# Kernel optimization log

Measured on AMD Instinct MI355X. Metric: run time of the kernel, lower is better.

The kernel has to match this reference:

```python
import jax, jax.numpy as jnp
import numpy as np

B, S, D, H = 2, 2048, 1024, 16
HD = D // H  # head_dim = 64
NEG = -1.0e9


def setup_inputs() -> dict:
    key = jax.random.key(0)
    ks = jax.random.split(key, 6)
    scale = 1.0 / np.sqrt(D)
    x = jax.random.normal(ks[0], (B, S, D), dtype=jnp.float32)
    # causal additive mask: 1.0 where position is masked (future), matching scores += mask * -1e9
    mask = jnp.triu(jnp.ones((S, S), dtype=jnp.float32), k=1)[None, None, :, :]
    wq = jax.random.normal(ks[1], (D, D), dtype=jnp.float32) * scale
    wk = jax.random.normal(ks[2], (D, D), dtype=jnp.float32) * scale
    wv = jax.random.normal(ks[3], (D, D), dtype=jnp.float32) * scale
    wo = jax.random.normal(ks[4], (D, D), dtype=jnp.float32) * scale
    z = jnp.zeros((D,), dtype=jnp.float32)
    return {"x": x, "mask": mask, "wq": wq, "bq": z, "wk": wk, "bk": z,
            "wv": wv, "bv": z, "wo": wo, "bo": z}


def _split_heads(t):
    # [B, S, D] -> [B, H, S, HD]
    return t.reshape(B, S, H, HD).transpose(0, 2, 1, 3)


def reference(x, mask, wq, bq, wk, bk, wv, bv, wo, bo):
    q = _split_heads(x @ wq + bq)
    k = _split_heads(x @ wk + bk)
    v = _split_heads(x @ wv + bv)
    inv_sqrt_d = 1.0 / jnp.sqrt(jnp.float32(HD))
    scores = jnp.einsum("bhqd,bhkd->bhqk", q, k) * inv_sqrt_d
    scores = scores + mask * NEG
    attn = jax.nn.softmax(scores, axis=-1)
    out = jnp.einsum("bhqk,bhkd->bhqd", attn, v)
    out = out.transpose(0, 2, 1, 3).reshape(B, S, D)  # merge heads
    return out @ wo + bo
```

## Files before the change

### kernel.cpp

```cpp
#include <hip/hip_runtime.h>
#include <hip/hip_bf16.h>


typedef __bf16 bf16x8 __attribute__((ext_vector_type(8)));
typedef __bf16 bf16x4 __attribute__((ext_vector_type(4)));
typedef float f32x4 __attribute__((ext_vector_type(4)));

#define S_LEN 2048
#define DMODEL 1024
#define NHEAD 16
#define HDIM 64
#define MROWS 4096

#define AS1 __attribute__((address_space(1)))
#define AS3 __attribute__((address_space(3)))

#define QSCALE 0.18033688f
#define LDP 136

__global__ void cast_x_kernel(const float* __restrict__ X, __bf16* __restrict__ Xb) {
    int i = (blockIdx.x * blockDim.x + threadIdx.x) * 4;
    float4 f = *(const float4*)&X[i];
    Xb[i + 0] = (__bf16)f.x;
    Xb[i + 1] = (__bf16)f.y;
    Xb[i + 2] = (__bf16)f.z;
    Xb[i + 3] = (__bf16)f.w;
}

__global__ void transpose_cast_kernel(
    const float* __restrict__ W0, const float* __restrict__ W1,
    const float* __restrict__ W2, const float* __restrict__ W3,
    __bf16* __restrict__ T0, __bf16* __restrict__ T1,
    __bf16* __restrict__ T2, __bf16* __restrict__ T3) {
    const float* W = (blockIdx.z == 0) ? W0 : (blockIdx.z == 1) ? W1 : (blockIdx.z == 2) ? W2 : W3;
    __bf16* WT = (blockIdx.z == 0) ? T0 : (blockIdx.z == 1) ? T1 : (blockIdx.z == 2) ? T2 : T3;
    __shared__ float tile[32][33];
    int bx = blockIdx.x, by = blockIdx.y;
    int tx = threadIdx.x;
    for (int i = threadIdx.y; i < 32; i += 8)
        tile[i][tx] = W[(size_t)(by * 32 + i) * DMODEL + bx * 32 + tx];
    __syncthreads();
    for (int i = threadIdx.y; i < 32; i += 8)
        WT[(size_t)(bx * 32 + i) * DMODEL + by * 32 + tx] = (__bf16)tile[tx][i];
}

__global__ __launch_bounds__(256) void gemm_qkv_kernel(
    const __bf16* __restrict__ X,
    const __bf16* __restrict__ WqT, const __bf16* __restrict__ WkT, const __bf16* __restrict__ WvT,
    const float* __restrict__ bq, const float* __restrict__ bk, const float* __restrict__ bv,
    __bf16* __restrict__ Q, __bf16* __restrict__ K, __bf16* __restrict__ Vt) {
    const int which = blockIdx.z;
    const __bf16* Bt = (which == 0) ? WqT : (which == 1) ? WkT : WvT;
    const float* bias = (which == 0) ? bq : (which == 1) ? bk : bv;
    __bf16* Out = (which == 0) ? Q : (which == 1) ? K : Vt;

    __shared__ alignas(16) __bf16 As[128 * 64];
    __shared__ alignas(16) __bf16 Bs[64 * 64];

    const int tid = threadIdx.x;
    const int lane = tid & 63;
    const int wave = tid >> 6;
    const int wm = wave >> 1, wn = wave & 1;
    const int quad = lane >> 4;
    const int l16 = lane & 15;
    const int m0 = blockIdx.x * 128;
    const int n0 = blockIdx.y * 64;
    const int r8 = lane >> 3;
    const int sc8 = ((lane & 7) ^ r8) * 8;
    const int gq0 = ((0 + quad) ^ (l16 & 7)) * 8;
    const int gq1 = ((4 + quad) ^ (l16 & 7)) * 8;

    f32x4 acc[4][2] = {};

    for (int k0 = 0; k0 < DMODEL; k0 += 64) {
        __syncthreads();
#pragma unroll
        for (int p = 0; p < 4; p++) {
            const int row = wave * 32 + p * 8;
            __builtin_amdgcn_global_load_lds(
                (const AS1 void*)&X[(size_t)(m0 + row + r8) * DMODEL + k0 + sc8],
                (AS3 void*)&As[row * 64], 16, 0, 0);
        }
#pragma unroll
        for (int p = 0; p < 2; p++) {
            const int row = wave * 16 + p * 8;
            __builtin_amdgcn_global_load_lds(
                (const AS1 void*)&Bt[(size_t)(n0 + row + r8) * DMODEL + k0 + sc8],
                (AS3 void*)&Bs[row * 64], 16, 0, 0);
        }
        __syncthreads();
#pragma unroll
        for (int ks = 0; ks < 2; ks++) {
            const int g = ks ? gq1 : gq0;
            bf16x8 af[4], bfr[2];
#pragma unroll
            for (int t = 0; t < 4; t++)
                af[t] = *(bf16x8*)&As[(wm * 64 + t * 16 + l16) * 64 + g];
#pragma unroll
            for (int t = 0; t < 2; t++)
                bfr[t] = *(bf16x8*)&Bs[(wn * 32 + t * 16 + l16) * 64 + g];
#pragma unroll
            for (int mt = 0; mt < 4; mt++)
#pragma unroll
                for (int nt = 0; nt < 2; nt++)
                    acc[mt][nt] = __builtin_amdgcn_mfma_f32_16x16x32_bf16(af[mt], bfr[nt], acc[mt][nt], 0, 0, 0);
        }
    }

#pragma unroll
    for (int mt = 0; mt < 4; mt++)
#pragma unroll
        for (int nt = 0; nt < 2; nt++) {
            const int n = n0 + wn * 32 + nt * 16 + l16;
            const float bn = bias[n];
            const int h = n >> 6, hd = n & 63;
            const int mbase = m0 + wm * 64 + mt * 16 + quad * 4;
            if (which == 2) {
                __bf16 pk[4];
#pragma unroll
                for (int r = 0; r < 4; r++) pk[r] = (__bf16)(acc[mt][nt][r] + bn);
                const int m = mbase;
                const int b = m >> 11, s = m & 2047;
                *(uint2*)&Out[(((size_t)(b * NHEAD + h) * HDIM + hd) * S_LEN) + s] = *(uint2*)pk;
            } else {
                const float sc = (which == 0) ? QSCALE : 1.0f;
#pragma unroll
                for (int r = 0; r < 4; r++) {
                    const int m = mbase + r;
                    const int b = m >> 11, s = m & 2047;
                    Out[(((size_t)(b * NHEAD + h) * S_LEN + s) * HDIM) + hd] =
                        (__bf16)((acc[mt][nt][r] + bn) * sc);
                }
            }
        }
}

__global__ __launch_bounds__(256) void gemm_out_kernel(
    const __bf16* __restrict__ A, const __bf16* __restrict__ Bt,
    const float* __restrict__ bias, float* __restrict__ Y) {
    __shared__ alignas(16) __bf16 As[64 * 64];
    __shared__ alignas(16) __bf16 Bs[64 * 64];

    const int tid = threadIdx.x;
    const int lane = tid & 63;
    const int wave = tid >> 6;
    const int wm = wave >> 1, wn = wave & 1;
    const int quad = lane >> 4;
    const int l16 = lane & 15;
    const int m0 = blockIdx.x * 64;
    const int n0 = blockIdx.y * 64;
    const int r8 = lane >> 3;
    const int sc8 = ((lane & 7) ^ r8) * 8;
    const int gq0 = ((0 + quad) ^ (l16 & 7)) * 8;
    const int gq1 = ((4 + quad) ^ (l16 & 7)) * 8;

    f32x4 acc[2][2] = {};

    for (int k0 = 0; k0 < DMODEL; k0 += 64) {
        __syncthreads();
#pragma unroll
        for (int p = 0; p < 2; p++) {
            const int row = wave * 16 + p * 8;
            __builtin_amdgcn_global_load_lds(
                (const AS1 void*)&A[(size_t)(m0 + row + r8) * DMODEL + k0 + sc8],
                (AS3 void*)&As[row * 64], 16, 0, 0);
            __builtin_amdgcn_global_load_lds(
                (const AS1 void*)&Bt[(size_t)(n0 + row + r8) * DMODEL + k0 + sc8],
                (AS3 void*)&Bs[row * 64], 16, 0, 0);
        }
        __syncthreads();
#pragma unroll
        for (int ks = 0; ks < 2; ks++) {
            const int g = ks ? gq1 : gq0;
            bf16x8 af[2], bfr[2];
#pragma unroll
            for (int t = 0; t < 2; t++) {
                af[t]  = *(bf16x8*)&As[(wm * 32 + t * 16 + l16) * 64 + g];
                bfr[t] = *(bf16x8*)&Bs[(wn * 32 + t * 16 + l16) * 64 + g];
            }
#pragma unroll
            for (int mt = 0; mt < 2; mt++)
#pragma unroll
                for (int nt = 0; nt < 2; nt++)
                    acc[mt][nt] = __builtin_amdgcn_mfma_f32_16x16x32_bf16(af[mt], bfr[nt], acc[mt][nt], 0, 0, 0);
        }
    }

#pragma unroll
    for (int mt = 0; mt < 2; mt++)
#pragma unroll
        for (int nt = 0; nt < 2; nt++)
#pragma unroll
            for (int r = 0; r < 4; r++) {
                int m = m0 + wm * 32 + mt * 16 + quad * 4 + r;
                int n = n0 + wn * 32 + nt * 16 + l16;
                Y[(size_t)m * DMODEL + n] = acc[mt][nt][r] + bias[n];
            }
}


template <int NT>
__device__ __forceinline__ void attn_tile(
    const __bf16* Ks, const __bf16* Vs, __bf16* Psw,
    const bf16x8& qf0, const bf16x8& qf1, const bf16x8& onef,
    f32x4 (&oacc)[4], f32x4& lacc,
    int q0, int k0, bool mask, int wave, int quad, int l16, int g0, int g1) {
    f32x4 sacc[NT];
#pragma unroll
    for (int nt = 0; nt < NT; nt++) sacc[nt] = (f32x4){0.f, 0.f, 0.f, 0.f};
#pragma unroll
    for (int nt = 0; nt < NT; nt++) {
        const int krow = (nt * 16 + l16) * 64;
        bf16x8 kf0 = *(bf16x8*)&Ks[krow + g0];
        bf16x8 kf1 = *(bf16x8*)&Ks[krow + g1];
        sacc[nt] = __builtin_amdgcn_mfma_f32_16x16x32_bf16(kf0, qf0, sacc[nt], 0, 0, 0);
        sacc[nt] = __builtin_amdgcn_mfma_f32_16x16x32_bf16(kf1, qf1, sacc[nt], 0, 0, 0);
    }
    const int qg = q0 + wave * 16 + l16;
    if (mask) {
#pragma unroll
        for (int nt = 0; nt < NT; nt++) {
            bf16x4 pv;
#pragma unroll
            for (int r = 0; r < 4; r++) {
                const int kcol = k0 + nt * 16 + quad * 4 + r;
                pv[r] = (__bf16)((kcol > qg) ? 0.0f : __builtin_amdgcn_exp2f(sacc[nt][r]));
            }
            *(bf16x4*)&Psw[l16 * LDP + nt * 16 + quad * 4] = pv;
        }
    } else {
#pragma unroll
        for (int nt = 0; nt < NT; nt++) {
            bf16x4 pv;
#pragma unroll
            for (int r = 0; r < 4; r++)
                pv[r] = (__bf16)__builtin_amdgcn_exp2f(sacc[nt][r]);
            *(bf16x4*)&Psw[l16 * LDP + nt * 16 + quad * 4] = pv;
        }
    }
#pragma unroll
    for (int ks = 0; ks < NT / 2; ks++) {
        bf16x8 pf = *(bf16x8*)&Psw[l16 * LDP + ks * 32 + quad * 8];
        const int vg = (((ks * 4 + quad) ^ (l16 & 7)) * 8);
#pragma unroll
        for (int nt2 = 0; nt2 < 4; nt2++) {
            bf16x8 vf = *(bf16x8*)&Vs[(nt2 * 16 + l16) * 128 + vg];
            oacc[nt2] = __builtin_amdgcn_mfma_f32_16x16x32_bf16(pf, vf, oacc[nt2], 0, 0, 0);
        }
        lacc = __builtin_amdgcn_mfma_f32_16x16x32_bf16(pf, onef, lacc, 0, 0, 0);
    }
}

__global__ __launch_bounds__(256, 3) void attn_kernel(
    const __bf16* __restrict__ Q, const __bf16* __restrict__ K, const __bf16* __restrict__ Vt,
    __bf16* __restrict__ Aout) {
    const int id = blockIdx.x;
    const int bh = id & 31;
    const int qt = 31 - (id >> 5);
    const int b = bh >> 4, h = bh & 15;
    const int tid = threadIdx.x, lane = tid & 63, wave = tid >> 6;
    const int quad = lane >> 4, l16 = lane & 15;

    __shared__ alignas(16) __bf16 Ks[128 * 64];
    __shared__ alignas(16) __bf16 Vs[64 * 128];
    __shared__ alignas(16) __bf16 Ps[4][16 * LDP];

    const size_t base = (size_t)bh * S_LEN * HDIM;
    const int q0 = qt * 64;
    const int qrow = q0 + wave * 16 + l16;

    bf16x8 qf0 = *(const bf16x8*)&Q[base + (size_t)qrow * HDIM + quad * 8];
    bf16x8 qf1 = *(const bf16x8*)&Q[base + (size_t)qrow * HDIM + 32 + quad * 8];

    bf16x8 onef;
#pragma unroll
    for (int jj = 0; jj < 8; jj++) onef[jj] = (__bf16)1.0f;

    f32x4 oacc[4] = {};
    f32x4 lacc = {};
    __bf16* Psw = &Ps[wave][0];

    const int r8k = lane >> 3;
    const int sck = ((lane & 7) ^ r8k) * 8;
    const int r4v = lane >> 4;
    const int g0 = (quad ^ (l16 & 7)) * 8;
    const int g1 = g0 ^ 32;

    const int kb_all = (qt >> 1) + 1;
    for (int kb = 0; kb < kb_all; kb++) {
        const int k0 = kb * 128;
        __syncthreads();
#pragma unroll
        for (int p = 0; p < 4; p++) {
            const int row = wave * 32 + p * 8;
            __builtin_amdgcn_global_load_lds(
                (const AS1 void*)&K[base + (size_t)(k0 + row + r8k) * HDIM + sck],
                (AS3 void*)&Ks[row * 64], 16, 0, 0);
        }
#pragma unroll
        for (int p = 0; p < 4; p++) {
            const int row = wave * 16 + p * 4;
            const int lc = ((lane & 15) ^ ((p * 4 + r4v) & 7)) * 8;
            __builtin_amdgcn_global_load_lds(
                (const AS1 void*)&Vt[base + (size_t)(row + r4v) * S_LEN + k0 + lc],
                (AS3 void*)&Vs[row * 128], 16, 0, 0);
        }
        __syncthreads();

        const bool last = (kb == kb_all - 1);
        if (!last)
            attn_tile<8>(Ks, Vs, Psw, qf0, qf1, onef, oacc, lacc, q0, k0, false,
                         wave, quad, l16, g0, g1);
        else if (qt & 1)
            attn_tile<8>(Ks, Vs, Psw, qf0, qf1, onef, oacc, lacc, q0, k0, true,
                         wave, quad, l16, g0, g1);
        else
            attn_tile<4>(Ks, Vs, Psw, qf0, qf1, onef, oacc, lacc, q0, k0, true,
                         wave, quad, l16, g0, g1);
    }

    float rl[4];
#pragma unroll
    for (int r = 0; r < 4; r++) rl[r] = 1.0f / lacc[r];
#pragma unroll
    for (int nt2 = 0; nt2 < 4; nt2++)
#pragma unroll
        for (int r = 0; r < 4; r++) {
            int qg = q0 + wave * 16 + quad * 4 + r;
            int col = h * HDIM + nt2 * 16 + l16;
            Aout[(size_t)(b * S_LEN + qg) * DMODEL + col] = (__bf16)(oacc[nt2][r] * rl[r]);
        }
}

extern "C" void kernel_launch(void* const* d_in, const int* in_sizes, int n_in,
                              void* d_out, int out_size, void* d_ws, size_t ws_size,
                              hipStream_t stream) {
    const float* x  = (const float*)d_in[0];
    const float* wq = (const float*)d_in[2];
    const float* bq = (const float*)d_in[3];
    const float* wk = (const float*)d_in[4];
    const float* bk = (const float*)d_in[5];
    const float* wv = (const float*)d_in[6];
    const float* bv = (const float*)d_in[7];
    const float* wo = (const float*)d_in[8];
    const float* bo = (const float*)d_in[9];
    float* out = (float*)d_out;

    char* ws = (char*)d_ws;
    __bf16* xb  = (__bf16*)(ws);
    __bf16* wqT = (__bf16*)(ws + ((size_t)8  << 20));
    __bf16* wkT = (__bf16*)(ws + ((size_t)10 << 20));
    __bf16* wvT = (__bf16*)(ws + ((size_t)12 << 20));
    __bf16* woT = (__bf16*)(ws + ((size_t)14 << 20));
    __bf16* Qb  = (__bf16*)(ws + ((size_t)16 << 20));
    __bf16* Kb  = (__bf16*)(ws + ((size_t)24 << 20));
    __bf16* Vtb = (__bf16*)(ws + ((size_t)32 << 20));
    __bf16* Ab  = (__bf16*)(ws + ((size_t)40 << 20));

    cast_x_kernel<<<4096, 256, 0, stream>>>(x, xb);
    transpose_cast_kernel<<<dim3(32, 32, 4), dim3(32, 8), 0, stream>>>(
        wq, wk, wv, wo, wqT, wkT, wvT, woT);
    gemm_qkv_kernel<<<dim3(32, 16, 3), 256, 0, stream>>>(xb, wqT, wkT, wvT, bq, bk, bv, Qb, Kb, Vtb);
    attn_kernel<<<1024, 256, 0, stream>>>(Qb, Kb, Vtb, Ab);
    gemm_out_kernel<<<dim3(64, 16), 256, 0, stream>>>(Ab, woT, bo, out);
}
```

Measured before the change: 183.7 us.

## Double-buffer 64-key K/V tiles in attention to overlap loads with compute

Shrinks the attention key block from 128 to 64 keys and double-buffers the K and V^T tiles in LDS. The next tile's global-to-LDS loads are issued before the current tile is computed, so memory latency overlaps MFMA work, with a single barrier per iteration. This doubles the number of loop iterations and barriers, and the smaller tile gives less work per barrier and less MFMA density per iteration. The LDS footprint stays about the same.

```diff
diff --git a/kernel.cpp b/kernel.cpp
--- a/kernel.cpp
+++ b/kernel.cpp
@@ -16,7 +16,7 @@
 #define AS3 __attribute__((address_space(3)))
 
 #define QSCALE 0.18033688f
-#define LDP 136
+#define LDP4 72
 
 __global__ void cast_x_kernel(const float* __restrict__ X, __bf16* __restrict__ Xb) {
     int i = (blockIdx.x * blockDim.x + threadIdx.x) * 4;
@@ -199,52 +199,44 @@
 }
 
 
-template <int NT>
-__device__ __forceinline__ void attn_tile(
+template <bool MASK>
+__device__ __forceinline__ void attn_tile64(
     const __bf16* Ks, const __bf16* Vs, __bf16* Psw,
     const bf16x8& qf0, const bf16x8& qf1, const bf16x8& onef,
     f32x4 (&oacc)[4], f32x4& lacc,
-    int q0, int k0, bool mask, int wave, int quad, int l16, int g0, int g1) {
-    f32x4 sacc[NT];
-#pragma unroll
-    for (int nt = 0; nt < NT; nt++) sacc[nt] = (f32x4){0.f, 0.f, 0.f, 0.f};
-#pragma unroll
-    for (int nt = 0; nt < NT; nt++) {
+    int qg, int k0, int quad, int l16, int g0, int g1) {
+    f32x4 sacc[4];
+#pragma unroll
+    for (int nt = 0; nt < 4; nt++) sacc[nt] = (f32x4){0.f, 0.f, 0.f, 0.f};
+#pragma unroll
+    for (int nt = 0; nt < 4; nt++) {
         const int krow = (nt * 16 + l16) * 64;
         bf16x8 kf0 = *(bf16x8*)&Ks[krow + g0];
         bf16x8 kf1 = *(bf16x8*)&Ks[krow + g1];
         sacc[nt] = __builtin_amdgcn_mfma_f32_16x16x32_bf16(kf0, qf0, sacc[nt], 0, 0, 0);
         sacc[nt] = __builtin_amdgcn_mfma_f32_16x16x32_bf16(kf1, qf1, sacc[nt], 0, 0, 0);
     }
-    const int qg = q0 + wave * 16 + l16;
-    if (mask) {
-#pragma unroll
-        for (int nt = 0; nt < NT; nt++) {
-            bf16x4 pv;
-#pragma unroll
-            for (int r = 0; r < 4; r++) {
+#pragma unroll
+    for (int nt = 0; nt < 4; nt++) {
+        bf16x4 pv;
+#pragma unroll
+        for (int r = 0; r < 4; r++) {
+            if (MASK) {
                 const int kcol = k0 + nt * 16 + quad * 4 + r;
                 pv[r] = (__bf16)((kcol > qg) ? 0.0f : __builtin_amdgcn_exp2f(sacc[nt][r]));
-            }
-            *(bf16x4*)&Psw[l16 * LDP + nt * 16 + quad * 4] = pv;
-        }
-    } else {
-#pragma unroll
-        for (int nt = 0; nt < NT; nt++) {
-            bf16x4 pv;
-#pragma unroll
-            for (int r = 0; r < 4; r++)
+            } else {
                 pv[r] = (__bf16)__builtin_amdgcn_exp2f(sacc[nt][r]);
-            *(bf16x4*)&Psw[l16 * LDP + nt * 16 + quad * 4] = pv;
-        }
-    }
-#pragma unroll
-    for (int ks = 0; ks < NT / 2; ks++) {
-        bf16x8 pf = *(bf16x8*)&Psw[l16 * LDP + ks * 32 + quad * 8];
+            }
+        }
+        *(bf16x4*)&Psw[l16 * LDP4 + nt * 16 + quad * 4] = pv;
+    }
+#pragma unroll
+    for (int ks = 0; ks < 2; ks++) {
+        bf16x8 pf = *(bf16x8*)&Psw[l16 * LDP4 + ks * 32 + quad * 8];
         const int vg = (((ks * 4 + quad) ^ (l16 & 7)) * 8);
 #pragma unroll
         for (int nt2 = 0; nt2 < 4; nt2++) {
-            bf16x8 vf = *(bf16x8*)&Vs[(nt2 * 16 + l16) * 128 + vg];
+            bf16x8 vf = *(bf16x8*)&Vs[(nt2 * 16 + l16) * 64 + vg];
             oacc[nt2] = __builtin_amdgcn_mfma_f32_16x16x32_bf16(pf, vf, oacc[nt2], 0, 0, 0);
         }
         lacc = __builtin_amdgcn_mfma_f32_16x16x32_bf16(pf, onef, lacc, 0, 0, 0);
@@ -261,9 +253,9 @@
     const int tid = threadIdx.x, lane = tid & 63, wave = tid >> 6;
     const int quad = lane >> 4, l16 = lane & 15;
 
-    __shared__ alignas(16) __bf16 Ks[128 * 64];
-    __shared__ alignas(16) __bf16 Vs[64 * 128];
-    __shared__ alignas(16) __bf16 Ps[4][16 * LDP];
+    __shared__ alignas(16) __bf16 Ks[2][64 * 64];
+    __shared__ alignas(16) __bf16 Vs[2][64 * 64];
+    __shared__ alignas(16) __bf16 Ps[4][16 * LDP4];
 
     const size_t base = (size_t)bh * S_LEN * HDIM;
     const int q0 = qt * 64;
@@ -282,41 +274,50 @@
 
     const int r8k = lane >> 3;
     const int sck = ((lane & 7) ^ r8k) * 8;
-    const int r4v = lane >> 4;
     const int g0 = (quad ^ (l16 & 7)) * 8;
     const int g1 = g0 ^ 32;
-
-    const int kb_all = (qt >> 1) + 1;
+    const int qg = q0 + wave * 16 + l16;
+
+    const int kb_all = qt + 1;
+
+#pragma unroll
+    for (int p = 0; p < 2; p++) {
+        const int row = wave * 16 + p * 8;
+        __builtin_amdgcn_global_load_lds(
+            (const AS1 void*)&K[base + (size_t)(row + r8k) * HDIM + sck],
+            (AS3 void*)&Ks[0][row * 64], 16, 0, 0);
+        __builtin_amdgcn_global_load_lds(
+            (const AS1 void*)&Vt[base + (size_t)(row + r8k) * S_LEN + sck],
+            (AS3 void*)&Vs[0][row * 64], 16, 0, 0);
+    }
+    __syncthreads();
+
+    int cur = 0;
     for (int kb = 0; kb < kb_all; kb++) {
-        const int k0 = kb * 128;
-        __syncthreads();
-#pragma unroll
-        for (int p = 0; p < 4; p++) {
-            const int row = wave * 32 + p * 8;
-            __builtin_amdgcn_global_load_lds(
-                (const AS1 void*)&K[base + (size_t)(k0 + row + r8k) * HDIM + sck],
-                (AS3 void*)&Ks[row * 64], 16, 0, 0);
-        }
-#pragma unroll
-        for (int p = 0; p < 4; p++) {
-            const int row = wave * 16 + p * 4;
-            const int lc = ((lane & 15) ^ ((p * 4 + r4v) & 7)) * 8;
-            __builtin_amdgcn_global_load_lds(
-                (const AS1 void*)&Vt[base + (size_t)(row + r4v) * S_LEN + k0 + lc],
-                (AS3 void*)&Vs[row * 128], 16, 0, 0);
-        }
-        __syncthreads();
-
-        const bool last = (kb == kb_all - 1);
-        if (!last)
-            attn_tile<8>(Ks, Vs, Psw, qf0, qf1, onef, oacc, lacc, q0, k0, false,
-                         wave, quad, l16, g0, g1);
-        else if (qt & 1)
-            attn_tile<8>(Ks, Vs, Psw, qf0, qf1, onef, oacc, lacc, q0, k0, true,
-                         wave, quad, l16, g0, g1);
+        if (kb + 1 < kb_all) {
+            const int k1 = (kb + 1) * 64;
+            const int nxt = cur ^ 1;
+#pragma unroll
+            for (int p = 0; p < 2; p++) {
+                const int row = wave * 16 + p * 8;
+                __builtin_amdgcn_global_load_lds(
+                    (const AS1 void*)&K[base + (size_t)(k1 + row + r8k) * HDIM + sck],
+                    (AS3 void*)&Ks[nxt][row * 64], 16, 0, 0);
+                __builtin_amdgcn_global_load_lds(
+                    (const AS1 void*)&Vt[base + (size_t)(row + r8k) * S_LEN + k1 + sck],
+                    (AS3 void*)&Vs[nxt][row * 64], 16, 0, 0);
+            }
+        }
+
+        const int k0 = kb * 64;
+        if (kb == kb_all - 1)
+            attn_tile64<true>(Ks[cur], Vs[cur], Psw, qf0, qf1, onef, oacc, lacc,
+                              qg, k0, quad, l16, g0, g1);
         else
-            attn_tile<4>(Ks, Vs, Psw, qf0, qf1, onef, oacc, lacc, q0, k0, true,
-                         wave, quad, l16, g0, g1);
+            attn_tile64<false>(Ks[cur], Vs[cur], Psw, qf0, qf1, onef, oacc, lacc,
+                               qg, k0, quad, l16, g0, g1);
+        __syncthreads();
+        cur ^= 1;
     }
 
     float rl[4];
@@ -326,9 +327,9 @@
     for (int nt2 = 0; nt2 < 4; nt2++)
 #pragma unroll
         for (int r = 0; r < 4; r++) {
-            int qg = q0 + wave * 16 + quad * 4 + r;
+            int qq = q0 + wave * 16 + quad * 4 + r;
             int col = h * HDIM + nt2 * 16 + l16;
-            Aout[(size_t)(b * S_LEN + qg) * DMODEL + col] = (__bf16)(oacc[nt2][r] * rl[r]);
+            Aout[(size_t)(b * S_LEN + qq) * DMODEL + col] = (__bf16)(oacc[nt2][r] * rl[r]);
         }
 }
 
```

New measurement: 186.1 us. Within noise of the previous version (+1.3%).

## Rewrite attention tile with 32x32 MFMA, split keys across waves, register P

Applied to the files above, without the earlier changes.

The attention inner loop switches from 16x16x32 MFMA to 32x32x16 MFMA. The four waves are split 2x2 over query rows and key halves, and the two key-half partial results are merged through shared memory at the end. P is packed to bf16 in registers and exchanged across lane halves with shuffles rather than staged through a per-wave LDS buffer, which removes the Ps buffer and its LDS traffic. The cost is a final LDS reduction with an extra sync, a different V swizzle, and loss of the half-tile shortcut on the masked diagonal tile, which is now always full width.

```diff
diff --git a/kernel.cpp b/kernel.cpp
--- a/kernel.cpp
+++ b/kernel.cpp
@@ -4,7 +4,10 @@
 
 typedef __bf16 bf16x8 __attribute__((ext_vector_type(8)));
 typedef __bf16 bf16x4 __attribute__((ext_vector_type(4)));
+typedef __bf16 bf16x2 __attribute__((ext_vector_type(2)));
 typedef float f32x4 __attribute__((ext_vector_type(4)));
+typedef float f32x16 __attribute__((ext_vector_type(16)));
+typedef unsigned int u32x4 __attribute__((ext_vector_type(4)));
 
 #define S_LEN 2048
 #define DMODEL 1024
@@ -16,7 +19,6 @@
 #define AS3 __attribute__((address_space(3)))
 
 #define QSCALE 0.18033688f
-#define LDP 136
 
 __global__ void cast_x_kernel(const float* __restrict__ X, __bf16* __restrict__ Xb) {
     int i = (blockIdx.x * blockDim.x + threadIdx.x) * 4;
@@ -199,55 +201,72 @@
 }
 
 
-template <int NT>
-__device__ __forceinline__ void attn_tile(
-    const __bf16* Ks, const __bf16* Vs, __bf16* Psw,
-    const bf16x8& qf0, const bf16x8& qf1, const bf16x8& onef,
-    f32x4 (&oacc)[4], f32x4& lacc,
-    int q0, int k0, bool mask, int wave, int quad, int l16, int g0, int g1) {
-    f32x4 sacc[NT];
-#pragma unroll
-    for (int nt = 0; nt < NT; nt++) sacc[nt] = (f32x4){0.f, 0.f, 0.f, 0.f};
-#pragma unroll
-    for (int nt = 0; nt < NT; nt++) {
-        const int krow = (nt * 16 + l16) * 64;
-        bf16x8 kf0 = *(bf16x8*)&Ks[krow + g0];
-        bf16x8 kf1 = *(bf16x8*)&Ks[krow + g1];
-        sacc[nt] = __builtin_amdgcn_mfma_f32_16x16x32_bf16(kf0, qf0, sacc[nt], 0, 0, 0);
-        sacc[nt] = __builtin_amdgcn_mfma_f32_16x16x32_bf16(kf1, qf1, sacc[nt], 0, 0, 0);
-    }
-    const int qg = q0 + wave * 16 + l16;
-    if (mask) {
-#pragma unroll
-        for (int nt = 0; nt < NT; nt++) {
-            bf16x4 pv;
-#pragma unroll
-            for (int r = 0; r < 4; r++) {
-                const int kcol = k0 + nt * 16 + quad * 4 + r;
-                pv[r] = (__bf16)((kcol > qg) ? 0.0f : __builtin_amdgcn_exp2f(sacc[nt][r]));
+static __device__ __forceinline__ unsigned pkbf2(float a, float b) {
+    bf16x2 t;
+    t[0] = (__bf16)a;
+    t[1] = (__bf16)b;
+    return __builtin_bit_cast(unsigned, t);
+}
+
+template <bool MASK>
+__device__ __forceinline__ void attn_tile32(
+    const __bf16* Ks, const __bf16* Vs,
+    const bf16x8 (&qf)[4], const bf16x8& onesf,
+    f32x16 (&oacc)[2], f32x16& lacc,
+    int q_lane, int kl0, int kabs0, int lane) {
+    const int l32 = lane & 31, hi = lane >> 5, l7 = lane & 7, l15 = lane & 15;
+    const int cbase = kl0 >> 3;
+    bf16x8 pa[4];
+#pragma unroll
+    for (int sub = 0; sub < 2; sub++) {
+        f32x16 s = {};
+        const int row = kl0 + sub * 32 + l32;
+#pragma unroll
+        for (int j = 0; j < 4; j++) {
+            const int ch = ((2 * j + hi) ^ l7) * 8;
+            bf16x8 kf = *(const bf16x8*)&Ks[row * 64 + ch];
+            s = __builtin_amdgcn_mfma_f32_32x32x16_bf16(kf, qf[j], s, 0, 0, 0);
+        }
+        float p[16];
+#pragma unroll
+        for (int r = 0; r < 16; r++) {
+            const float e = __builtin_amdgcn_exp2f(s[r]);
+            if (MASK) {
+                const int kabs = kabs0 + sub * 32 + (r & 3) + 8 * (r >> 2) + 4 * hi;
+                p[r] = (kabs > q_lane) ? 0.0f : e;
+            } else {
+                p[r] = e;
             }
-            *(bf16x4*)&Psw[l16 * LDP + nt * 16 + quad * 4] = pv;
-        }
-    } else {
-#pragma unroll
-        for (int nt = 0; nt < NT; nt++) {
-            bf16x4 pv;
-#pragma unroll
-            for (int r = 0; r < 4; r++)
-                pv[r] = (__bf16)__builtin_amdgcn_exp2f(sacc[nt][r]);
-            *(bf16x4*)&Psw[l16 * LDP + nt * 16 + quad * 4] = pv;
-        }
-    }
-#pragma unroll
-    for (int ks = 0; ks < NT / 2; ks++) {
-        bf16x8 pf = *(bf16x8*)&Psw[l16 * LDP + ks * 32 + quad * 8];
-        const int vg = (((ks * 4 + quad) ^ (l16 & 7)) * 8);
-#pragma unroll
-        for (int nt2 = 0; nt2 < 4; nt2++) {
-            bf16x8 vf = *(bf16x8*)&Vs[(nt2 * 16 + l16) * 128 + vg];
-            oacc[nt2] = __builtin_amdgcn_mfma_f32_16x16x32_bf16(pf, vf, oacc[nt2], 0, 0, 0);
-        }
-        lacc = __builtin_amdgcn_mfma_f32_16x16x32_bf16(pf, onef, lacc, 0, 0, 0);
+        }
+        const unsigned c0 = pkbf2(p[0], p[1]),   c1 = pkbf2(p[2], p[3]);
+        const unsigned c2 = pkbf2(p[4], p[5]),   c3 = pkbf2(p[6], p[7]);
+        const unsigned c4 = pkbf2(p[8], p[9]),   c5 = pkbf2(p[10], p[11]);
+        const unsigned c6 = pkbf2(p[12], p[13]), c7 = pkbf2(p[14], p[15]);
+        const unsigned sA0 = hi ? c0 : c2, sA1 = hi ? c1 : c3;
+        const unsigned rA0 = __shfl_xor(sA0, 32, 64), rA1 = __shfl_xor(sA1, 32, 64);
+        const unsigned sB0 = hi ? c4 : c6, sB1 = hi ? c5 : c7;
+        const unsigned rB0 = __shfl_xor(sB0, 32, 64), rB1 = __shfl_xor(sB1, 32, 64);
+        u32x4 wA, wB;
+        if (hi) {
+            wA[0] = rA0; wA[1] = rA1; wA[2] = c2; wA[3] = c3;
+            wB[0] = rB0; wB[1] = rB1; wB[2] = c6; wB[3] = c7;
+        } else {
+            wA[0] = c0; wA[1] = c1; wA[2] = rA0; wA[3] = rA1;
+            wB[0] = c4; wB[1] = c5; wB[2] = rB0; wB[3] = rB1;
+        }
+        pa[sub * 2]     = __builtin_bit_cast(bf16x8, wA);
+        pa[sub * 2 + 1] = __builtin_bit_cast(bf16x8, wB);
+    }
+#pragma unroll
+    for (int kblk = 0; kblk < 4; kblk++) {
+#pragma unroll
+        for (int dsub = 0; dsub < 2; dsub++) {
+            const int hd = dsub * 32 + l32;
+            const int ch = ((cbase + kblk * 2 + hi) ^ l15) * 8;
+            bf16x8 vf = *(const bf16x8*)&Vs[hd * 128 + ch];
+            oacc[dsub] = __builtin_amdgcn_mfma_f32_32x32x16_bf16(pa[kblk], vf, oacc[dsub], 0, 0, 0);
+        }
+        lacc = __builtin_amdgcn_mfma_f32_32x32x16_bf16(pa[kblk], onesf, lacc, 0, 0, 0);
     }
 }
 
@@ -259,34 +278,36 @@
     const int qt = 31 - (id >> 5);
     const int b = bh >> 4, h = bh & 15;
     const int tid = threadIdx.x, lane = tid & 63, wave = tid >> 6;
-    const int quad = lane >> 4, l16 = lane & 15;
-
-    __shared__ alignas(16) __bf16 Ks[128 * 64];
-    __shared__ alignas(16) __bf16 Vs[64 * 128];
-    __shared__ alignas(16) __bf16 Ps[4][16 * LDP];
+    const int wq = wave >> 1, wk = wave & 1;
+    const int l32 = lane & 31, hi = lane >> 5;
+
+    __shared__ alignas(16) __bf16 SMEM[128 * 64 + 64 * 128];
+    __bf16* Ks = SMEM;
+    __bf16* Vs = SMEM + 128 * 64;
 
     const size_t base = (size_t)bh * S_LEN * HDIM;
     const int q0 = qt * 64;
-    const int qrow = q0 + wave * 16 + l16;
-
-    bf16x8 qf0 = *(const bf16x8*)&Q[base + (size_t)qrow * HDIM + quad * 8];
-    bf16x8 qf1 = *(const bf16x8*)&Q[base + (size_t)qrow * HDIM + 32 + quad * 8];
-
-    bf16x8 onef;
-#pragma unroll
-    for (int jj = 0; jj < 8; jj++) onef[jj] = (__bf16)1.0f;
-
-    f32x4 oacc[4] = {};
-    f32x4 lacc = {};
-    __bf16* Psw = &Ps[wave][0];
+    const int q_lane = q0 + wq * 32 + l32;
+
+    bf16x8 qf[4];
+#pragma unroll
+    for (int j = 0; j < 4; j++)
+        qf[j] = *(const bf16x8*)&Q[base + (size_t)q_lane * HDIM + j * 16 + hi * 8];
+
+    bf16x8 onesf;
+#pragma unroll
+    for (int jj = 0; jj < 8; jj++) onesf[jj] = (__bf16)1.0f;
+
+    f32x16 oacc[2] = {};
+    f32x16 lacc = {};
 
     const int r8k = lane >> 3;
     const int sck = ((lane & 7) ^ r8k) * 8;
     const int r4v = lane >> 4;
-    const int g0 = (quad ^ (l16 & 7)) * 8;
-    const int g1 = g0 ^ 32;
 
     const int kb_all = (qt >> 1) + 1;
+    const int kl0 = wk * 64;
+
     for (int kb = 0; kb < kb_all; kb++) {
         const int k0 = kb * 128;
         __syncthreads();
@@ -300,36 +321,50 @@
 #pragma unroll
         for (int p = 0; p < 4; p++) {
             const int row = wave * 16 + p * 4;
-            const int lc = ((lane & 15) ^ ((p * 4 + r4v) & 7)) * 8;
+            const int lc = ((lane & 15) ^ ((p * 4 + r4v) & 15)) * 8;
             __builtin_amdgcn_global_load_lds(
                 (const AS1 void*)&Vt[base + (size_t)(row + r4v) * S_LEN + k0 + lc],
                 (AS3 void*)&Vs[row * 128], 16, 0, 0);
         }
         __syncthreads();
 
-        const bool last = (kb == kb_all - 1);
-        if (!last)
-            attn_tile<8>(Ks, Vs, Psw, qf0, qf1, onef, oacc, lacc, q0, k0, false,
-                         wave, quad, l16, g0, g1);
-        else if (qt & 1)
-            attn_tile<8>(Ks, Vs, Psw, qf0, qf1, onef, oacc, lacc, q0, k0, true,
-                         wave, quad, l16, g0, g1);
+        if (kb == kb_all - 1)
+            attn_tile32<true>(Ks, Vs, qf, onesf, oacc, lacc, q_lane, kl0, k0 + kl0, lane);
         else
-            attn_tile<4>(Ks, Vs, Psw, qf0, qf1, onef, oacc, lacc, q0, k0, true,
-                         wave, quad, l16, g0, g1);
-    }
-
-    float rl[4];
-#pragma unroll
-    for (int r = 0; r < 4; r++) rl[r] = 1.0f / lacc[r];
-#pragma unroll
-    for (int nt2 = 0; nt2 < 4; nt2++)
-#pragma unroll
-        for (int r = 0; r < 4; r++) {
-            int qg = q0 + wave * 16 + quad * 4 + r;
-            int col = h * HDIM + nt2 * 16 + l16;
-            Aout[(size_t)(b * S_LEN + qg) * DMODEL + col] = (__bf16)(oacc[nt2][r] * rl[r]);
-        }
+            attn_tile32<false>(Ks, Vs, qf, onesf, oacc, lacc, q_lane, kl0, k0 + kl0, lane);
+    }
+
+    __syncthreads();
+    float* scr = (float*)SMEM;
+    const int slot = (wq * 64 + lane) * 49;
+    if (wk) {
+#pragma unroll
+        for (int ss = 0; ss < 2; ss++)
+#pragma unroll
+            for (int r = 0; r < 16; r++) scr[slot + ss * 16 + r] = oacc[ss][r];
+#pragma unroll
+        for (int r = 0; r < 16; r++) scr[slot + 32 + r] = lacc[r];
+    }
+    __syncthreads();
+    if (!wk) {
+#pragma unroll
+        for (int ss = 0; ss < 2; ss++)
+#pragma unroll
+            for (int r = 0; r < 16; r++) oacc[ss][r] += scr[slot + ss * 16 + r];
+#pragma unroll
+        for (int r = 0; r < 16; r++) lacc[r] += scr[slot + 32 + r];
+        float rl[16];
+#pragma unroll
+        for (int r = 0; r < 16; r++) rl[r] = 1.0f / lacc[r];
+#pragma unroll
+        for (int ss = 0; ss < 2; ss++)
+#pragma unroll
+            for (int r = 0; r < 16; r++) {
+                const int q = q0 + wq * 32 + (r & 3) + 8 * (r >> 2) + 4 * hi;
+                Aout[(size_t)(b * S_LEN + q) * DMODEL + h * 64 + ss * 32 + l32] =
+                    (__bf16)(oacc[ss][r] * rl[r]);
+            }
+    }
 }
 
 extern "C" void kernel_launch(void* const* d_in, const int* in_sizes, int n_in,
```

Result: no change. 183.6 us (-0.1%).
